# Optimization experiments

Measured on AMD Instinct MI355X. Metric: run time of the kernel, lower is better.

## Reference

```python
import jax, jax.numpy as jnp
import numpy as np
import math

B, T, C = 2, 2048, 1024
H = 16            # n_head
RATIO = 4         # ratio_kv
HKV = H // RATIO  # n_head_kv = 4
HD = C // H       # head_dim = 64
G = H // HKV      # query heads per kv head = 4


def _alibi_slopes(n_heads):
    # n_heads must be a power of 2 here (H=16)
    assert math.log2(n_heads).is_integer()
    start = 2.0 ** (-(2.0 ** (-(math.log2(n_heads) - 3))))
    return np.array([start * (start ** i) for i in range(n_heads)], dtype=np.float32)


def setup_inputs() -> dict:
    key = jax.random.key(0)
    ks = jax.random.split(key, 5)
    return {
        "x": jax.random.normal(ks[0], (B, T, C), dtype=jnp.float32),
        "Wq": jax.random.normal(ks[1], (C, C), dtype=jnp.float32) * 0.02,
        "Wk": jax.random.normal(ks[2], (C, HKV * HD), dtype=jnp.float32) * 0.02,
        "Wv": jax.random.normal(ks[3], (C, HKV * HD), dtype=jnp.float32) * 0.02,
        "Wo": jax.random.normal(ks[4], (C, C), dtype=jnp.float32) * 0.02,
    }


def reference(x, Wq, Wk, Wv, Wo):
    # GQA causal attention with ALiBi bias (flash-disabled fallback path).
    # q: [B,HKV,G,T,HD] (grouped query heads), k/v: [B,HKV,T,HD]
    q = (x @ Wq).reshape(B, T, H, HD).transpose(0, 2, 1, 3).reshape(B, HKV, G, T, HD)
    k = (x @ Wk).reshape(B, T, HKV, HD).transpose(0, 2, 1, 3)
    v = (x @ Wv).reshape(B, T, HKV, HD).transpose(0, 2, 1, 3)

    scale = 1.0 / math.sqrt(HD)
    att = jnp.einsum('bkgtd,bksd->bkgts', q, k) * scale  # [B,HKV,G,T,T]

    # ALiBi: original repeats alibi(n_head) by G and truncates to n_head,
    # so query head h uses slope get_slopes(H)[h // G] == slopes[:HKV] per kv group.
    slopes = jnp.asarray(_alibi_slopes(H))[:HKV]          # [HKV]
    pos = jnp.arange(T)
    rel = (pos[None, :] - pos[:, None]).astype(jnp.float32)  # [T,T], rel[i,j]=j-i
    bias = slopes[:, None, None] * rel                    # [HKV,T,T]
    causal = jnp.triu(jnp.full((T, T), -jnp.inf, dtype=jnp.float32), 1)

    att = att + bias[None, :, None] + causal
    att = jax.nn.softmax(att.astype(jnp.float32), axis=-1).astype(q.dtype)

    y = jnp.einsum('bkgts,bksd->bkgtd', att, v)           # [B,HKV,G,T,HD]
    y = y.reshape(B, H, T, HD).transpose(0, 2, 1, 3).reshape(B, T, C)
    return y @ Wo
```

## Files before the change

### kernel.cpp

```cpp
#include <hip/hip_runtime.h>
#include <hip/hip_bf16.h>
#include <math.h>

#define B_ 2
#define T_ 2048
#define C_ 1024
#define H_ 16
#define HKV_ 4
#define G_ 4
#define HD_ 64
#define KVC_ 256
#define NQKV_ 1536
#define NQT_ 32

typedef __attribute__((ext_vector_type(8))) short bf16x8;
typedef __attribute__((ext_vector_type(4))) float f32x4;

static __device__ inline short f2bf(float f) {
    __hip_bfloat16 h = __float2bfloat16(f);
    short s;
    __builtin_memcpy(&s, &h, 2);
    return s;
}
static __device__ inline short f2bf_trunc(float f) {
    unsigned int u;
    __builtin_memcpy(&u, &f, 4);
    return (short)(u >> 16);
}
static __device__ inline float bf2f(short s) {
    unsigned int u = ((unsigned int)(unsigned short)s) << 16;
    float f;
    __builtin_memcpy(&f, &u, 4);
    return f;
}

static __device__ inline void gload_lds16(const short* g, short* lds) {
    __builtin_amdgcn_global_load_lds(
        (const __attribute__((address_space(1))) unsigned int*)g,
        (__attribute__((address_space(3))) unsigned int*)lds, 16, 0, 0);
}

__global__ __launch_bounds__(256) void cast_bf16(
    const float* __restrict__ in, short* __restrict__ out, int n)
{
    const int i = (blockIdx.x * 256 + threadIdx.x) * 8;
    if (i >= n) return;
    const float4 a = *(const float4*)(in + i);
    const float4 b = *(const float4*)(in + i + 4);
    bf16x8 o;
    o[0] = f2bf(a.x); o[1] = f2bf(a.y); o[2] = f2bf(a.z); o[3] = f2bf(a.w);
    o[4] = f2bf(b.x); o[5] = f2bf(b.y); o[6] = f2bf(b.z); o[7] = f2bf(b.w);
    *(bf16x8*)(out + i) = o;
}

__global__ __launch_bounds__(256) void w_transpose(
    const float* __restrict__ Wq, const float* __restrict__ Wk,
    const float* __restrict__ Wv, const float* __restrict__ Wo,
    short* __restrict__ Wt, short* __restrict__ Wot)
{
    const int z = blockIdx.z;
    const float* in;
    short* out;
    int N;
    if (z == 0)      { in = Wq; out = Wt;                     N = C_; }
    else if (z == 1) { in = Wk; out = Wt + C_ * C_;           N = KVC_; }
    else if (z == 2) { in = Wv; out = Wt + (C_ + KVC_) * C_;  N = KVC_; }
    else             { in = Wo; out = Wot;                    N = C_; }
    const int n0 = blockIdx.x * 32;
    if (n0 >= N) return;
    __shared__ float t[32][33];
    const int tx = threadIdx.x, ty = threadIdx.y;
    const int k0 = blockIdx.y * 32;
    #pragma unroll
    for (int j = 0; j < 4; j++)
        t[ty + j * 8][tx] = in[(size_t)(k0 + ty + j * 8) * N + n0 + tx];
    __syncthreads();
    #pragma unroll
    for (int j = 0; j < 4; j++)
        out[(size_t)(n0 + ty + j * 8) * C_ + k0 + tx] = f2bf(t[tx][ty + j * 8]);
}

template <bool OUT_BF16>
__global__ __launch_bounds__(256) void gemm_bf16(
    const short* __restrict__ A, const short* __restrict__ Bt,
    void* __restrict__ Cout, int M, int N, int K)
{
    __shared__ short As[3][64 * 32];
    __shared__ short Bs[3][128 * 32];
    const int tid = threadIdx.x;
    const int wave = tid >> 6, lane = tid & 63;
    const int l15 = lane & 15, quad = lane >> 4;

    const int gx = gridDim.x;
    const int nwg = gx * gridDim.y;
    int bid = blockIdx.y * gx + blockIdx.x;
    bid = (bid & 7) * (nwg >> 3) + (bid >> 3);
    const int row0 = (bid / gx) * 64, col0 = (bid % gx) * 128;

    const int wr = (wave >> 1) * 32, wc = (wave & 1) * 64;
    const int sr = lane >> 2, kof = (lane & 3) * 8;

    f32x4 acc[2][4];
    #pragma unroll
    for (int i = 0; i < 2; i++)
        #pragma unroll
        for (int j = 0; j < 4; j++)
            acc[i][j] = (f32x4){0.f, 0.f, 0.f, 0.f};

#define GSTAGE(KT, BUF) do {                                                   \
        gload_lds16(A + (size_t)(row0 + wave * 16 + sr) * K + (KT) + kof,      \
                    &As[BUF][wave * 512]);                                     \
        gload_lds16(Bt + (size_t)(col0 + (wave * 2) * 16 + sr) * K + (KT) + kof,\
                    &Bs[BUF][(wave * 2) * 512]);                               \
        gload_lds16(Bt + (size_t)(col0 + (wave * 2 + 1) * 16 + sr) * K + (KT) + kof,\
                    &Bs[BUF][(wave * 2 + 1) * 512]);                           \
    } while (0)

    GSTAGE(0, 0);
    GSTAGE(32, 1);
    asm volatile("s_waitcnt vmcnt(3)" ::: "memory");
    __builtin_amdgcn_s_barrier();

    const int nkt = K >> 5;
    int cur = 0, nxt = 2;
    for (int t = 0; t < nkt; ++t) {
        if (t + 2 < nkt) GSTAGE((t + 2) * 32, nxt);

        bf16x8 af[2], bfr[4];
        #pragma unroll
        for (int mt = 0; mt < 2; mt++)
            af[mt] = *(const bf16x8*)&As[cur][(wr + mt * 16 + l15) * 32 + quad * 8];
        #pragma unroll
        for (int nt = 0; nt < 4; nt++)
            bfr[nt] = *(const bf16x8*)&Bs[cur][(wc + nt * 16 + l15) * 32 + quad * 8];
        #pragma unroll
        for (int mt = 0; mt < 2; mt++)
            #pragma unroll
            for (int nt = 0; nt < 4; nt++)
                acc[mt][nt] = __builtin_amdgcn_mfma_f32_16x16x32_bf16(
                    af[mt], bfr[nt], acc[mt][nt], 0, 0, 0);

        if (t + 2 < nkt)
            asm volatile("s_waitcnt vmcnt(3)" ::: "memory");
        else
            asm volatile("s_waitcnt vmcnt(0)" ::: "memory");
        __builtin_amdgcn_s_barrier();
        cur = (cur == 2) ? 0 : cur + 1;
        nxt = (nxt == 2) ? 0 : nxt + 1;
    }
#undef GSTAGE

    #pragma unroll
    for (int mt = 0; mt < 2; mt++) {
        #pragma unroll
        for (int r = 0; r < 4; r++) {
            const size_t row = row0 + wr + mt * 16 + quad * 4 + r;
            #pragma unroll
            for (int nt = 0; nt < 4; nt++) {
                const size_t col = col0 + wc + nt * 16 + l15;
                if (OUT_BF16)
                    ((short*)Cout)[row * N + col] = f2bf(acc[mt][nt][r]);
                else
                    ((float*)Cout)[row * N + col] = acc[mt][nt][r];
            }
        }
    }
}

__global__ __launch_bounds__(256) void kv_tile(
    const short* __restrict__ QKV, short* __restrict__ Kt, short* __restrict__ Vt)
{
    __shared__ short Ls[64 * 72];
    const int jt = blockIdx.x;
    const int bk = blockIdx.y;
    const int b = bk >> 2, kh = bk & 3;
    const int tid = threadIdx.x;
    const int key = tid >> 2, d16 = (tid & 3) * 16;
    const size_t src = (size_t)(b * T_ + jt * 64 + key) * NQKV_ + C_ + kh * 64 + d16;
    const size_t tbase = (size_t)(bk * 32 + jt) * 4096;

    {
        const int i = (key >> 4) * 2 + (d16 >> 5);
        const int qd = (d16 & 31) >> 3;
        short* dst = Kt + tbase + i * 512 + (qd * 16 + (key & 15)) * 8;
        *(bf16x8*)dst         = *(const bf16x8*)(QKV + src);
        *(bf16x8*)(dst + 128) = *(const bf16x8*)(QKV + src + 8);
    }
    *(bf16x8*)&Ls[key * 72 + d16]     = *(const bf16x8*)(QKV + src + KVC_);
    *(bf16x8*)&Ls[key * 72 + d16 + 8] = *(const bf16x8*)(QKV + src + KVC_ + 8);
    __syncthreads();
    const int d = tid >> 2, k16 = (tid & 3) * 16;
    bf16x8 o0, o1;
    #pragma unroll
    for (int i = 0; i < 8; i++) o0[i] = Ls[(k16 + i) * 72 + d];
    #pragma unroll
    for (int i = 0; i < 8; i++) o1[i] = Ls[(k16 + 8 + i) * 72 + d];
    {
        const int i = (d >> 4) * 2 + (k16 >> 5);
        const int qk = (k16 & 31) >> 3;
        short* dst = Vt + tbase + i * 512 + (qk * 16 + (d & 15)) * 8;
        *(bf16x8*)dst         = o0;
        *(bf16x8*)(dst + 128) = o1;
    }
}

#define LSTR 72

#define ATTN_ITER(J, SCURH, SCURL, SNXTH, SNXTL)                               \
  {                                                                            \
    const int j_ = (J);                                                        \
    const bool doL_ = (j_ <= qtL);                                             \
                                                     \
    {                                                                          \
        const float base = slope2 * (float)(j_ * 64 + l15 - quad * 4 - qrow0H);\
        if (j_ == qtH) {                                                       \
            _Pragma("unroll")                                                  \
            for (int nt = 0; nt < 4; nt++) {                                   \
                const int colsw = ((nt * 16 + l15) ^ wswz);                    \
                _Pragma("unroll")                                              \
                for (int r = 0; r < 4; r++) {                                  \
                    const float relv = (float)(j_ * 64 + l15 - quad * 4 - qrow0H)\
                                     + (float)(nt * 16 - r);                   \
                    float p = __builtin_amdgcn_exp2f(                          \
                        fmaf(slope2, (float)(nt * 16 - r), base) + SCURH[nt][r]);\
                    if (relv > 0.f) p = 0.f;                                   \
                    Pw[(quad * 4 + r) * LSTR + colsw] = f2bf_trunc(p);         \
                }                                                              \
            }                                                                  \
        } else {                                                               \
            _Pragma("unroll")                                                  \
            for (int nt = 0; nt < 4; nt++) {                                   \
                const int colsw = ((nt * 16 + l15) ^ wswz);                    \
                _Pragma("unroll")                                              \
                for (int r = 0; r < 4; r++) {                                  \
                    float p = __builtin_amdgcn_exp2f(                          \
                        fmaf(slope2, (float)(nt * 16 - r), base) + SCURH[nt][r]);\
                    Pw[(quad * 4 + r) * LSTR + colsw] = f2bf_trunc(p);         \
                }                                                              \
            }                                                                  \
        }                                                                      \
    }                                                                          \
    if (doL_) {                                                                \
        const float base = slope2 * (float)(j_ * 64 + l15 - quad * 4 - qrow0L);\
        if (j_ == qtL) {                                                       \
            _Pragma("unroll")                                                  \
            for (int nt = 0; nt < 4; nt++) {                                   \
                const int colsw = ((nt * 16 + l15) ^ wswz);                    \
                _Pragma("unroll")                                              \
                for (int r = 0; r < 4; r++) {                                  \
                    const float relv = (float)(j_ * 64 + l15 - quad * 4 - qrow0L)\
                                     + (float)(nt * 16 - r);                   \
                    float p = __builtin_amdgcn_exp2f(                          \
                        fmaf(slope2, (float)(nt * 16 - r), base) + SCURL[nt][r]);\
                    if (relv > 0.f) p = 0.f;                                   \
                    Pw[(16 + quad * 4 + r) * LSTR + colsw] = f2bf_trunc(p);    \
                }                                                              \
            }                                                                  \
        } else {                                                               \
            _Pragma("unroll")                                                  \
            for (int nt = 0; nt < 4; nt++) {                                   \
                const int colsw = ((nt * 16 + l15) ^ wswz);                    \
                _Pragma("unroll")                                              \
                for (int r = 0; r < 4; r++) {                                  \
                    float p = __builtin_amdgcn_exp2f(                          \
                        fmaf(slope2, (float)(nt * 16 - r), base) + SCURL[nt][r]);\
                    Pw[(16 + quad * 4 + r) * LSTR + colsw] = f2bf_trunc(p);    \
                }                                                              \
            }                                                                  \
        }                                                                      \
    }                                                                          \
                    \
    if (j_ < qtH) {                                                            \
        const bool doLn_ = (j_ + 1 <= qtL);                                    \
        __builtin_amdgcn_s_setprio(1);                                         \
        _Pragma("unroll")                                                      \
        for (int nt = 0; nt < 4; nt++) {                                       \
            f32x4 a = {0.f, 0.f, 0.f, 0.f};                                    \
            a = __builtin_amdgcn_mfma_f32_16x16x32_bf16(qfH[0], kf[nt*2+0], a, 0, 0, 0);\
            a = __builtin_amdgcn_mfma_f32_16x16x32_bf16(qfH[1], kf[nt*2+1], a, 0, 0, 0);\
            SNXTH[nt] = a;                                                     \
        }                                                                      \
        if (doLn_) {                                                           \
            _Pragma("unroll")                                                  \
            for (int nt = 0; nt < 4; nt++) {                                   \
                f32x4 a = {0.f, 0.f, 0.f, 0.f};                                \
                a = __builtin_amdgcn_mfma_f32_16x16x32_bf16(qfL[0], kf[nt*2+0], a, 0, 0, 0);\
                a = __builtin_amdgcn_mfma_f32_16x16x32_bf16(qfL[1], kf[nt*2+1], a, 0, 0, 0);\
                SNXTL[nt] = a;                                                 \
            }                                                                  \
        }                                                                      \
        __builtin_amdgcn_s_setprio(0);                                         \
        const int pk_ = (j_ + 2 <= qtH) ? j_ + 2 : qtH;                        \
        _Pragma("unroll")                                                      \
        for (int i = 0; i < 8; i++)                                            \
            kf[i] = *(const bf16x8*)(Kt + (size_t)pk_ * 4096 + i * 512 + lane * 8);\
    }                                                                          \
    __asm__ volatile("s_waitcnt lgkmcnt(0)" ::: "memory");                     \
                                            \
    {                                                                          \
        bf16x8 pf0 = *(const bf16x8*)&Pw[l15 * LSTR + ((quad * 8) ^ rswz)];    \
        bf16x8 pf1 = *(const bf16x8*)&Pw[l15 * LSTR + ((32 + quad * 8) ^ rswz)];\
        __builtin_amdgcn_s_setprio(1);                                         \
        laccH = __builtin_amdgcn_mfma_f32_16x16x32_bf16(pf0, ones, laccH, 0, 0, 0);\
        laccH = __builtin_amdgcn_mfma_f32_16x16x32_bf16(pf1, ones, laccH, 0, 0, 0);\
        _Pragma("unroll")                                                      \
        for (int nt = 0; nt < 4; nt++) {                                       \
            OaccH[nt] = __builtin_amdgcn_mfma_f32_16x16x32_bf16(               \
                pf0, vf[nt*2+0], OaccH[nt], 0, 0, 0);                          \
            OaccH[nt] = __builtin_amdgcn_mfma_f32_16x16x32_bf16(               \
                pf1, vf[nt*2+1], OaccH[nt], 0, 0, 0);                          \
        }                                                                      \
        __builtin_amdgcn_s_setprio(0);                                         \
    }                                                                          \
    if (doL_) {                                                                \
        bf16x8 pf0 = *(const bf16x8*)&Pw[(16 + l15) * LSTR + ((quad * 8) ^ rswz)];\
        bf16x8 pf1 = *(const bf16x8*)&Pw[(16 + l15) * LSTR + ((32 + quad * 8) ^ rswz)];\
        __builtin_amdgcn_s_setprio(1);                                         \
        laccL = __builtin_amdgcn_mfma_f32_16x16x32_bf16(pf0, ones, laccL, 0, 0, 0);\
        laccL = __builtin_amdgcn_mfma_f32_16x16x32_bf16(pf1, ones, laccL, 0, 0, 0);\
        _Pragma("unroll")                                                      \
        for (int nt = 0; nt < 4; nt++) {                                       \
            OaccL[nt] = __builtin_amdgcn_mfma_f32_16x16x32_bf16(               \
                pf0, vf[nt*2+0], OaccL[nt], 0, 0, 0);                          \
            OaccL[nt] = __builtin_amdgcn_mfma_f32_16x16x32_bf16(               \
                pf1, vf[nt*2+1], OaccL[nt], 0, 0, 0);                          \
        }                                                                      \
        __builtin_amdgcn_s_setprio(0);                                         \
    }                                                                          \
    const int pv_ = (j_ + 1 <= qtH) ? j_ + 1 : qtH;                            \
    _Pragma("unroll")                                                          \
    for (int i = 0; i < 8; i++)                                                \
        vf[i] = *(const bf16x8*)(Vt + (size_t)pv_ * 4096 + i * 512 + lane * 8);\
  }

__global__ __launch_bounds__(256, 2) void attn_mfma(
    const short* __restrict__ QKV, const short* __restrict__ Ktg,
    const short* __restrict__ Vtg, short* __restrict__ Y)
{
    const int qx = blockIdx.x;
    const int bh = blockIdx.y;
    const int qtL = qx, qtH = NQT_ - 1 - qx;
    const int b = bh >> 4, h = bh & 15, kh = h >> 2;
    const float slope2 = exp2f(-0.5f * (float)(kh + 1)) * 1.44269504f;
    const int tid = threadIdx.x;
    const int wave = tid >> 6, lane = tid & 63;
    const int l15 = lane & 15, quad = lane >> 4;

    __shared__ short Ps[4 * 32 * LSTR];
    short* Pw = &Ps[wave * 32 * LSTR];
    const int wswz = ((quad >> 1) & 1) << 4;
    const int rswz = ((l15 >> 3) & 1) << 4;

    const size_t bT = (size_t)b * T_;
    const size_t tb0 = (size_t)((b * HKV_ + kh) * 32) * 4096;
    const short* Kt = Ktg + tb0;
    const short* Vt = Vtg + tb0;
    const int qrow0H = qtH * 64 + wave * 16;
    const int qrow0L = qtL * 64 + wave * 16;

    const float qscale = 0.125f * 1.44269504f;
    bf16x8 qfH[2], qfL[2];
    #pragma unroll
    for (int k0 = 0; k0 < 2; k0++) {
        const short* qpH = QKV + (bT + qrow0H + l15) * NQKV_ + h * 64;
        const short* qpL = QKV + (bT + qrow0L + l15) * NQKV_ + h * 64;
        bf16x8 rH = *(const bf16x8*)(qpH + k0 * 32 + quad * 8);
        bf16x8 rL = *(const bf16x8*)(qpL + k0 * 32 + quad * 8);
        #pragma unroll
        for (int j = 0; j < 8; j++) {
            qfH[k0][j] = f2bf(bf2f(rH[j]) * qscale);
            qfL[k0][j] = f2bf(bf2f(rL[j]) * qscale);
        }
    }

    const short one_s = (short)0x3F80;
    const bf16x8 ones = {one_s, one_s, one_s, one_s, one_s, one_s, one_s, one_s};

    f32x4 OaccH[4], OaccL[4], laccH, laccL;
    #pragma unroll
    for (int nt = 0; nt < 4; nt++) {
        OaccH[nt] = (f32x4){0.f, 0.f, 0.f, 0.f};
        OaccL[nt] = (f32x4){0.f, 0.f, 0.f, 0.f};
    }
    laccH = (f32x4){0.f, 0.f, 0.f, 0.f};
    laccL = (f32x4){0.f, 0.f, 0.f, 0.f};

    bf16x8 kf[8], vf[8];
    #pragma unroll
    for (int i = 0; i < 8; i++)
        kf[i] = *(const bf16x8*)(Kt + i * 512 + lane * 8);
    #pragma unroll
    for (int i = 0; i < 8; i++)
        vf[i] = *(const bf16x8*)(Vt + i * 512 + lane * 8);

    f32x4 sAH[4], sAL[4], sBH[4], sBL[4];
    #pragma unroll
    for (int nt = 0; nt < 4; nt++) {
        f32x4 a = {0.f, 0.f, 0.f, 0.f};
        a = __builtin_amdgcn_mfma_f32_16x16x32_bf16(qfH[0], kf[nt*2+0], a, 0, 0, 0);
        a = __builtin_amdgcn_mfma_f32_16x16x32_bf16(qfH[1], kf[nt*2+1], a, 0, 0, 0);
        sAH[nt] = a;
    }
    #pragma unroll
    for (int nt = 0; nt < 4; nt++) {
        f32x4 a = {0.f, 0.f, 0.f, 0.f};
        a = __builtin_amdgcn_mfma_f32_16x16x32_bf16(qfL[0], kf[nt*2+0], a, 0, 0, 0);
        a = __builtin_amdgcn_mfma_f32_16x16x32_bf16(qfL[1], kf[nt*2+1], a, 0, 0, 0);
        sAL[nt] = a;
    }
    {
        #pragma unroll
        for (int i = 0; i < 8; i++)
            kf[i] = *(const bf16x8*)(Kt + (size_t)4096 + i * 512 + lane * 8);
    }

    for (int j = 0; j <= qtH; j += 2) {
        ATTN_ITER(j, sAH, sAL, sBH, sBL);
        if (j + 1 <= qtH)
            ATTN_ITER(j + 1, sBH, sBL, sAH, sAL);
    }

    #pragma unroll
    for (int r = 0; r < 4; r++) {
        const float invH = 1.f / laccH[r];
        const float invL = 1.f / laccL[r];
        const int rowH = qrow0H + quad * 4 + r;
        const int rowL = qrow0L + quad * 4 + r;
        short* ypH = Y + (bT + rowH) * C_ + h * 64 + l15;
        short* ypL = Y + (bT + rowL) * C_ + h * 64 + l15;
        #pragma unroll
        for (int nt = 0; nt < 4; nt++) {
            ypH[nt * 16] = f2bf(OaccH[nt][r] * invH);
            ypL[nt * 16] = f2bf(OaccL[nt][r] * invL);
        }
    }
}

extern "C" void kernel_launch(void* const* d_in, const int* in_sizes, int n_in,
                              void* d_out, int out_size, void* d_ws, size_t ws_size,
                              hipStream_t stream) {
    const float* x  = (const float*)d_in[0];
    const float* Wq = (const float*)d_in[1];
    const float* Wk = (const float*)d_in[2];
    const float* Wv = (const float*)d_in[3];
    const float* Wo = (const float*)d_in[4];
    float* out = (float*)d_out;

    const int M = B_ * T_;
    short* xb  = (short*)d_ws;
    short* Wt  = xb  + (size_t)M * C_;
    short* Wot = Wt  + (size_t)NQKV_ * C_;
    short* QKV = Wot + (size_t)C_ * C_;
    short* Yb  = QKV + (size_t)M * NQKV_;
    short* Ktg = Yb  + (size_t)M * C_;
    short* Vtg = Ktg + (size_t)8 * 32 * 4096;

    cast_bf16<<<dim3(M * C_ / (256 * 8)), dim3(256), 0, stream>>>(x, xb, M * C_);
    w_transpose<<<dim3(32, 32, 4), dim3(32, 8), 0, stream>>>(Wq, Wk, Wv, Wo, Wt, Wot);

    gemm_bf16<true><<<dim3(NQKV_ / 128, M / 64), dim3(256), 0, stream>>>(
        xb, Wt, QKV, M, NQKV_, C_);
    kv_tile<<<dim3(32, 8), dim3(256), 0, stream>>>(QKV, Ktg, Vtg);
    attn_mfma<<<dim3(NQT_ / 2, B_ * H_), dim3(256), 0, stream>>>(QKV, Ktg, Vtg, Yb);
    gemm_bf16<false><<<dim3(C_ / 128, M / 64), dim3(256), 0, stream>>>(
        Yb, Wot, out, M, C_, C_);
}
```

Before: 164.5 us.

## Process two KV tiles per iteration with double-buffered P and K/V registers

Restructures the attention main loop so each iteration handles two KV tiles. Both QK score tiles are computed and written through softmax into separate LDS buffers before a single LDS wait and two batched PV accumulations. It drops the software-pipelined QK-ahead scheme and the s_setprio hints in favour of doubled K/V register buffers prefetched two tiles ahead. The aim is fewer LDS waits and more independent work between memory loads, at the cost of more registers (four K/V fragment sets) and double the LDS for P, which may reduce occupancy under the launch bounds.

```diff
diff --git a/kernel.cpp b/kernel.cpp
--- a/kernel.cpp
+++ b/kernel.cpp
@@ -206,25 +206,39 @@
 
 #define LSTR 72
 
-#define ATTN_ITER(J, SCURH, SCURL, SNXTH, SNXTL)                               \
-  {                                                                            \
-    const int j_ = (J);                                                        \
-    const bool doL_ = (j_ <= qtL);                                             \
-                                                     \
-    {                                                                          \
-        const float base = slope2 * (float)(j_ * 64 + l15 - quad * 4 - qrow0H);\
-        if (j_ == qtH) {                                                       \
+#define QK_TILE(KF, SH, SL, DOL)                                               \
+  { _Pragma("unroll")                                                          \
+    for (int nt = 0; nt < 4; nt++) {                                           \
+        f32x4 a = {0.f, 0.f, 0.f, 0.f};                                        \
+        a = __builtin_amdgcn_mfma_f32_16x16x32_bf16(qfH[0], KF[nt*2+0], a, 0, 0, 0);\
+        a = __builtin_amdgcn_mfma_f32_16x16x32_bf16(qfH[1], KF[nt*2+1], a, 0, 0, 0);\
+        SH[nt] = a;                                                            \
+    }                                                                          \
+    if (DOL) {                                                                 \
+        _Pragma("unroll")                                                      \
+        for (int nt = 0; nt < 4; nt++) {                                       \
+            f32x4 a = {0.f, 0.f, 0.f, 0.f};                                    \
+            a = __builtin_amdgcn_mfma_f32_16x16x32_bf16(qfL[0], KF[nt*2+0], a, 0, 0, 0);\
+            a = __builtin_amdgcn_mfma_f32_16x16x32_bf16(qfL[1], KF[nt*2+1], a, 0, 0, 0);\
+            SL[nt] = a;                                                        \
+        }                                                                      \
+    } }
+
+#define SMAX_TILE(J, SH, SL, DOL, PW)                                          \
+  { {                                                                          \
+        const float base_ = slope2 * (float)((J) * 64 + l15 - quad * 4 - qrow0H);\
+        if ((J) == qtH) {                                                      \
             _Pragma("unroll")                                                  \
             for (int nt = 0; nt < 4; nt++) {                                   \
                 const int colsw = ((nt * 16 + l15) ^ wswz);                    \
                 _Pragma("unroll")                                              \
                 for (int r = 0; r < 4; r++) {                                  \
-                    const float relv = (float)(j_ * 64 + l15 - quad * 4 - qrow0H)\
+                    const float relv = (float)((J) * 64 + l15 - quad * 4 - qrow0H)\
                                      + (float)(nt * 16 - r);                   \
                     float p = __builtin_amdgcn_exp2f(                          \
-                        fmaf(slope2, (float)(nt * 16 - r), base) + SCURH[nt][r]);\
+                        fmaf(slope2, (float)(nt * 16 - r), base_) + SH[nt][r]);\
                     if (relv > 0.f) p = 0.f;                                   \
-                    Pw[(quad * 4 + r) * LSTR + colsw] = f2bf_trunc(p);         \
+                    PW[(quad * 4 + r) * LSTR + colsw] = f2bf_trunc(p);         \
                 }                                                              \
             }                                                                  \
         } else {                                                               \
@@ -234,26 +248,26 @@
                 _Pragma("unroll")                                              \
                 for (int r = 0; r < 4; r++) {                                  \
                     float p = __builtin_amdgcn_exp2f(                          \
-                        fmaf(slope2, (float)(nt * 16 - r), base) + SCURH[nt][r]);\
-                    Pw[(quad * 4 + r) * LSTR + colsw] = f2bf_trunc(p);         \
+                        fmaf(slope2, (float)(nt * 16 - r), base_) + SH[nt][r]);\
+                    PW[(quad * 4 + r) * LSTR + colsw] = f2bf_trunc(p);         \
                 }                                                              \
             }                                                                  \
         }                                                                      \
     }                                                                          \
-    if (doL_) {                                                                \
-        const float base = slope2 * (float)(j_ * 64 + l15 - quad * 4 - qrow0L);\
-        if (j_ == qtL) {                                                       \
+    if (DOL) {                                                                 \
+        const float base_ = slope2 * (float)((J) * 64 + l15 - quad * 4 - qrow0L);\
+        if ((J) == qtL) {                                                      \
             _Pragma("unroll")                                                  \
             for (int nt = 0; nt < 4; nt++) {                                   \
                 const int colsw = ((nt * 16 + l15) ^ wswz);                    \
                 _Pragma("unroll")                                              \
                 for (int r = 0; r < 4; r++) {                                  \
-                    const float relv = (float)(j_ * 64 + l15 - quad * 4 - qrow0L)\
+                    const float relv = (float)((J) * 64 + l15 - quad * 4 - qrow0L)\
                                      + (float)(nt * 16 - r);                   \
                     float p = __builtin_amdgcn_exp2f(                          \
-                        fmaf(slope2, (float)(nt * 16 - r), base) + SCURL[nt][r]);\
+                        fmaf(slope2, (float)(nt * 16 - r), base_) + SL[nt][r]);\
                     if (relv > 0.f) p = 0.f;                                   \
-                    Pw[(16 + quad * 4 + r) * LSTR + colsw] = f2bf_trunc(p);    \
+                    PW[(16 + quad * 4 + r) * LSTR + colsw] = f2bf_trunc(p);    \
                 }                                                              \
             }                                                                  \
         } else {                                                               \
@@ -263,75 +277,40 @@
                 _Pragma("unroll")                                              \
                 for (int r = 0; r < 4; r++) {                                  \
                     float p = __builtin_amdgcn_exp2f(                          \
-                        fmaf(slope2, (float)(nt * 16 - r), base) + SCURL[nt][r]);\
-                    Pw[(16 + quad * 4 + r) * LSTR + colsw] = f2bf_trunc(p);    \
+                        fmaf(slope2, (float)(nt * 16 - r), base_) + SL[nt][r]);\
+                    PW[(16 + quad * 4 + r) * LSTR + colsw] = f2bf_trunc(p);    \
                 }                                                              \
             }                                                                  \
         }                                                                      \
-    }                                                                          \
-                    \
-    if (j_ < qtH) {                                                            \
-        const bool doLn_ = (j_ + 1 <= qtL);                                    \
-        __builtin_amdgcn_s_setprio(1);                                         \
-        _Pragma("unroll")                                                      \
-        for (int nt = 0; nt < 4; nt++) {                                       \
-            f32x4 a = {0.f, 0.f, 0.f, 0.f};                                    \
-            a = __builtin_amdgcn_mfma_f32_16x16x32_bf16(qfH[0], kf[nt*2+0], a, 0, 0, 0);\
-            a = __builtin_amdgcn_mfma_f32_16x16x32_bf16(qfH[1], kf[nt*2+1], a, 0, 0, 0);\
-            SNXTH[nt] = a;                                                     \
-        }                                                                      \
-        if (doLn_) {                                                           \
-            _Pragma("unroll")                                                  \
-            for (int nt = 0; nt < 4; nt++) {                                   \
-                f32x4 a = {0.f, 0.f, 0.f, 0.f};                                \
-                a = __builtin_amdgcn_mfma_f32_16x16x32_bf16(qfL[0], kf[nt*2+0], a, 0, 0, 0);\
-                a = __builtin_amdgcn_mfma_f32_16x16x32_bf16(qfL[1], kf[nt*2+1], a, 0, 0, 0);\
-                SNXTL[nt] = a;                                                 \
-            }                                                                  \
-        }                                                                      \
-        __builtin_amdgcn_s_setprio(0);                                         \
-        const int pk_ = (j_ + 2 <= qtH) ? j_ + 2 : qtH;                        \
-        _Pragma("unroll")                                                      \
-        for (int i = 0; i < 8; i++)                                            \
-            kf[i] = *(const bf16x8*)(Kt + (size_t)pk_ * 4096 + i * 512 + lane * 8);\
-    }                                                                          \
-    __asm__ volatile("s_waitcnt lgkmcnt(0)" ::: "memory");                     \
-                                            \
-    {                                                                          \
-        bf16x8 pf0 = *(const bf16x8*)&Pw[l15 * LSTR + ((quad * 8) ^ rswz)];    \
-        bf16x8 pf1 = *(const bf16x8*)&Pw[l15 * LSTR + ((32 + quad * 8) ^ rswz)];\
-        __builtin_amdgcn_s_setprio(1);                                         \
+    } }
+
+#define PV_TILE(PW, VF, DOL)                                                   \
+  { {                                                                          \
+        bf16x8 pf0 = *(const bf16x8*)&PW[l15 * LSTR + ((quad * 8) ^ rswz)];    \
+        bf16x8 pf1 = *(const bf16x8*)&PW[l15 * LSTR + ((32 + quad * 8) ^ rswz)];\
         laccH = __builtin_amdgcn_mfma_f32_16x16x32_bf16(pf0, ones, laccH, 0, 0, 0);\
         laccH = __builtin_amdgcn_mfma_f32_16x16x32_bf16(pf1, ones, laccH, 0, 0, 0);\
         _Pragma("unroll")                                                      \
         for (int nt = 0; nt < 4; nt++) {                                       \
             OaccH[nt] = __builtin_amdgcn_mfma_f32_16x16x32_bf16(               \
-                pf0, vf[nt*2+0], OaccH[nt], 0, 0, 0);                          \
+                pf0, VF[nt*2+0], OaccH[nt], 0, 0, 0);                          \
             OaccH[nt] = __builtin_amdgcn_mfma_f32_16x16x32_bf16(               \
-                pf1, vf[nt*2+1], OaccH[nt], 0, 0, 0);                          \
+                pf1, VF[nt*2+1], OaccH[nt], 0, 0, 0);                          \
         }                                                                      \
-        __builtin_amdgcn_s_setprio(0);                                         \
     }                                                                          \
-    if (doL_) {                                                                \
-        bf16x8 pf0 = *(const bf16x8*)&Pw[(16 + l15) * LSTR + ((quad * 8) ^ rswz)];\
-        bf16x8 pf1 = *(const bf16x8*)&Pw[(16 + l15) * LSTR + ((32 + quad * 8) ^ rswz)];\
-        __builtin_amdgcn_s_setprio(1);                                         \
+    if (DOL) {                                                                 \
+        bf16x8 pf0 = *(const bf16x8*)&PW[(16 + l15) * LSTR + ((quad * 8) ^ rswz)];\
+        bf16x8 pf1 = *(const bf16x8*)&PW[(16 + l15) * LSTR + ((32 + quad * 8) ^ rswz)];\
         laccL = __builtin_amdgcn_mfma_f32_16x16x32_bf16(pf0, ones, laccL, 0, 0, 0);\
         laccL = __builtin_amdgcn_mfma_f32_16x16x32_bf16(pf1, ones, laccL, 0, 0, 0);\
         _Pragma("unroll")                                                      \
         for (int nt = 0; nt < 4; nt++) {                                       \
             OaccL[nt] = __builtin_amdgcn_mfma_f32_16x16x32_bf16(               \
-                pf0, vf[nt*2+0], OaccL[nt], 0, 0, 0);                          \
+                pf0, VF[nt*2+0], OaccL[nt], 0, 0, 0);                          \
             OaccL[nt] = __builtin_amdgcn_mfma_f32_16x16x32_bf16(               \
-                pf1, vf[nt*2+1], OaccL[nt], 0, 0, 0);                          \
+                pf1, VF[nt*2+1], OaccL[nt], 0, 0, 0);                          \
         }                                                                      \
-        __builtin_amdgcn_s_setprio(0);                                         \
-    }                                                                          \
-    const int pv_ = (j_ + 1 <= qtH) ? j_ + 1 : qtH;                            \
-    _Pragma("unroll")                                                          \
-    for (int i = 0; i < 8; i++)                                                \
-        vf[i] = *(const bf16x8*)(Vt + (size_t)pv_ * 4096 + i * 512 + lane * 8);\
-  }
+    } }
 
 __global__ __launch_bounds__(256, 2) void attn_mfma(
     const short* __restrict__ QKV, const short* __restrict__ Ktg,
@@ -347,7 +326,9 @@
     const int l15 = lane & 15, quad = lane >> 4;
 
     __shared__ short Ps[4 * 32 * LSTR];
-    short* Pw = &Ps[wave * 32 * LSTR];
+    __shared__ short Ps2[4 * 32 * LSTR];
+    short* Pw  = &Ps[wave * 32 * LSTR];
+    short* Pw2 = &Ps2[wave * 32 * LSTR];
     const int wswz = ((quad >> 1) & 1) << 4;
     const int rswz = ((l15 >> 3) & 1) << 4;
 
@@ -385,39 +366,50 @@
     laccH = (f32x4){0.f, 0.f, 0.f, 0.f};
     laccL = (f32x4){0.f, 0.f, 0.f, 0.f};
 
-    bf16x8 kf[8], vf[8];
-    #pragma unroll
-    for (int i = 0; i < 8; i++)
-        kf[i] = *(const bf16x8*)(Kt + i * 512 + lane * 8);
-    #pragma unroll
-    for (int i = 0; i < 8; i++)
-        vf[i] = *(const bf16x8*)(Vt + i * 512 + lane * 8);
-
-    f32x4 sAH[4], sAL[4], sBH[4], sBL[4];
-    #pragma unroll
-    for (int nt = 0; nt < 4; nt++) {
-        f32x4 a = {0.f, 0.f, 0.f, 0.f};
-        a = __builtin_amdgcn_mfma_f32_16x16x32_bf16(qfH[0], kf[nt*2+0], a, 0, 0, 0);
-        a = __builtin_amdgcn_mfma_f32_16x16x32_bf16(qfH[1], kf[nt*2+1], a, 0, 0, 0);
-        sAH[nt] = a;
-    }
-    #pragma unroll
-    for (int nt = 0; nt < 4; nt++) {
-        f32x4 a = {0.f, 0.f, 0.f, 0.f};
-        a = __builtin_amdgcn_mfma_f32_16x16x32_bf16(qfL[0], kf[nt*2+0], a, 0, 0, 0);
-        a = __builtin_amdgcn_mfma_f32_16x16x32_bf16(qfL[1], kf[nt*2+1], a, 0, 0, 0);
-        sAL[nt] = a;
-    }
-    {
-        #pragma unroll
-        for (int i = 0; i < 8; i++)
-            kf[i] = *(const bf16x8*)(Kt + (size_t)4096 + i * 512 + lane * 8);
+    bf16x8 kfA[8], vfA[8], kfB[8], vfB[8];
+    #pragma unroll
+    for (int i = 0; i < 8; i++) {
+        kfA[i] = *(const bf16x8*)(Kt + i * 512 + lane * 8);
+        vfA[i] = *(const bf16x8*)(Vt + i * 512 + lane * 8);
+        kfB[i] = *(const bf16x8*)(Kt + 4096 + i * 512 + lane * 8);
+        vfB[i] = *(const bf16x8*)(Vt + 4096 + i * 512 + lane * 8);
     }
 
     for (int j = 0; j <= qtH; j += 2) {
-        ATTN_ITER(j, sAH, sAL, sBH, sBL);
-        if (j + 1 <= qtH)
-            ATTN_ITER(j + 1, sBH, sBL, sAH, sAL);
+        const bool have2 = (j + 1 <= qtH);
+        const bool doL1 = (j <= qtL);
+        const bool doL2 = (j + 1 <= qtL);
+        const int pk1 = (j + 2 <= qtH) ? j + 2 : qtH;
+        const int pk2 = (j + 3 <= qtH) ? j + 3 : qtH;
+
+        {
+            f32x4 sH1[4], sL1[4];
+            QK_TILE(kfA, sH1, sL1, doL1);
+            #pragma unroll
+            for (int i = 0; i < 8; i++)
+                kfA[i] = *(const bf16x8*)(Kt + (size_t)pk1 * 4096 + i * 512 + lane * 8);
+            SMAX_TILE(j, sH1, sL1, doL1, Pw);
+        }
+        if (have2) {
+            f32x4 sH2[4], sL2[4];
+            QK_TILE(kfB, sH2, sL2, doL2);
+            #pragma unroll
+            for (int i = 0; i < 8; i++)
+                kfB[i] = *(const bf16x8*)(Kt + (size_t)pk2 * 4096 + i * 512 + lane * 8);
+            SMAX_TILE(j + 1, sH2, sL2, doL2, Pw2);
+        }
+
+        __asm__ volatile("s_waitcnt lgkmcnt(0)" ::: "memory");
+
+        PV_TILE(Pw, vfA, doL1);
+        if (have2)
+            PV_TILE(Pw2, vfB, doL2);
+
+        #pragma unroll
+        for (int i = 0; i < 8; i++) {
+            vfA[i] = *(const bf16x8*)(Vt + (size_t)pk1 * 4096 + i * 512 + lane * 8);
+            vfB[i] = *(const bf16x8*)(Vt + (size_t)pk2 * 4096 + i * 512 + lane * 8);
+        }
     }
 
     #pragma unroll
```

After: 178.2 us. 8.3% more time.
